# Performance work log

Measured on AMD Instinct MI355X. Metric: run time of the kernel, lower is better.

Reference implementation:

```python
import jax, jax.numpy as jnp
import numpy as np

N_NODES, N_EDGES, N_GRAPHS = 30000, 70000, 1024
TOWERS, F_IN, F_OUT, N_LAYERS = 5, 75, 15, 4
DEG_HIST = np.array([0.0, 100.0, 400.0, 300.0, 50.0], dtype=np.float32)
AVG_DEG_LOG = float((np.log(np.arange(len(DEG_HIST)) + 1.0) * DEG_HIST).sum() / DEG_HIST.sum())


def setup_inputs():
    key = jax.random.key(0)
    ks = jax.random.split(key, 16)
    g = lambda k, shp, fan: jax.random.normal(k, shp, jnp.float32) * (1.0 / np.sqrt(fan))
    return dict(
        x=jax.random.randint(ks[0], (N_NODES,), 0, 21),
        edge_index=jax.random.randint(ks[1], (2, N_EDGES), 0, N_NODES),
        edge_attr=jax.random.randint(ks[2], (N_EDGES,), 0, 4),
        batch=jnp.sort(jax.random.randint(ks[3], (N_NODES,), 0, N_GRAPHS)),
        node_emb=g(ks[4], (21, 75), 75),
        edge_emb=g(ks[5], (4, 50), 50),
        enc_w=g(ks[6], (N_LAYERS, 50, 75), 50),
        enc_b=jnp.zeros((N_LAYERS, 75), jnp.float32),
        pre_w=g(ks[7], (N_LAYERS, TOWERS, 3 * F_IN, F_IN), 3 * F_IN),
        pre_b=jnp.zeros((N_LAYERS, TOWERS, F_IN), jnp.float32),
        post_w=g(ks[8], (N_LAYERS, TOWERS, 13 * F_IN, F_OUT), 13 * F_IN),
        post_b=jnp.zeros((N_LAYERS, TOWERS, F_OUT), jnp.float32),
        lin_w=g(ks[9], (N_LAYERS, 75, 75), 75),
        lin_b=jnp.zeros((N_LAYERS, 75), jnp.float32),
        bn_g=jnp.ones((N_LAYERS, 75), jnp.float32),
        bn_b=jnp.zeros((N_LAYERS, 75), jnp.float32),
        mlp_w1=g(ks[10], (75, 50), 75), mlp_b1=jnp.zeros((50,), jnp.float32),
        mlp_w2=g(ks[11], (50, 25), 50), mlp_b2=jnp.zeros((25,), jnp.float32),
        mlp_w3=g(ks[12], (25, 1), 25), mlp_b3=jnp.zeros((1,), jnp.float32),
    )


def _pna_layer(h, src, dst, e_enc, pw, pb, qw, qb, lw, lb):
    n = h.shape[0]
    # message: cat[x_i, x_j, edge_enc] shared across towers, per-tower pre-NN
    msg = jnp.concatenate([h[dst], h[src], e_enc], axis=-1)            # [E, 3*F_in]
    m = jnp.einsum('ef,tfo->eto', msg, pw) + pb                        # [E, T, F_in]
    deg = jax.ops.segment_sum(jnp.ones((m.shape[0],), m.dtype), dst, n)
    has = (deg > 0)[:, None, None]
    cnt = jnp.maximum(deg, 1.0)[:, None, None]                         # clamp(1)
    mean = jax.ops.segment_sum(m, dst, n) / cnt
    mean_sq = jax.ops.segment_sum(m * m, dst, n) / cnt
    std = jnp.sqrt(jax.nn.relu(mean_sq - mean * mean) + 1e-5)
    mn = jnp.where(has, jax.ops.segment_min(m, dst, n), 0.0)
    mx = jnp.where(has, jax.ops.segment_max(m, dst, n), 0.0)
    agg = jnp.concatenate([mean, mn, mx, std], axis=-1)                # [N, T, 4*F_in]
    amp = jnp.log(cnt + 1.0) / AVG_DEG_LOG                             # amplification scaler
    scaled = jnp.concatenate([agg, agg * amp, agg / amp], axis=-1)     # [N, T, 12*F_in]
    post_in = jnp.concatenate(
        [jnp.broadcast_to(h[:, None, :], (n, TOWERS, F_IN)), scaled], axis=-1)  # [N, T, 13*F_in]
    out = jnp.einsum('ntf,tfo->nto', post_in, qw) + qb                 # [N, T, F_out]
    return out.reshape(n, TOWERS * F_OUT) @ lw + lb                    # [N, 75]


def _bn_relu(h, g, b):
    mu = h.mean(axis=0)
    var = h.var(axis=0)
    return jax.nn.relu((h - mu) * jax.lax.rsqrt(var + 1e-5) * g + b)


def reference(x, edge_index, edge_attr, batch, node_emb, edge_emb, enc_w, enc_b,
              pre_w, pre_b, post_w, post_b, lin_w, lin_b, bn_g, bn_b,
              mlp_w1, mlp_b1, mlp_w2, mlp_b2, mlp_w3, mlp_b3):
    h = node_emb[x]                      # [N, 75]
    e = edge_emb[edge_attr]              # [E, 50]
    src, dst = edge_index[0], edge_index[1]
    for l in range(N_LAYERS):
        e_enc = e @ enc_w[l] + enc_b[l]  # [E, 75]
        h = _bn_relu(_pna_layer(h, src, dst, e_enc, pre_w[l], pre_b[l],
                                post_w[l], post_b[l], lin_w[l], lin_b[l]),
                     bn_g[l], bn_b[l])
    hg = jax.ops.segment_sum(h, batch, N_GRAPHS)   # global_add_pool -> [G, 75]
    z = jax.nn.relu(hg @ mlp_w1 + mlp_b1)
    z = jax.nn.relu(z @ mlp_w2 + mlp_b2)
    return z @ mlp_w3 + mlp_b3
```

## Files before the change

kernel.cpp:

```cpp
#include <hip/hip_runtime.h>
#include <hip/hip_bf16.h>
#include <float.h>
#include <math.h>

#define NN 30000
#define NE 70000
#define NG 1024
#define NT 5
#define FI 75
#define NL 4

#define AMP_DENOM 1.1824939264481302f

#define ABW 832
#define AGW 1600
#define HBW 96
#define SBH 328

typedef __attribute__((ext_vector_type(8))) short bf16x8;
typedef __attribute__((ext_vector_type(4))) float f32x4;

__device__ __forceinline__ float bf2f(unsigned short u) {
    return __uint_as_float(((unsigned int)u) << 16);
}
__device__ __forceinline__ unsigned short f2bf(float f) {
    __hip_bfloat16 h = __float2bfloat16(f);
    return *reinterpret_cast<unsigned short*>(&h);
}

__global__ __launch_bounds__(256) void k_deg(const int* __restrict__ dst, int* __restrict__ deg) {
    int e = blockIdx.x * 256 + threadIdx.x;
    if (e < NE) atomicAdd(&deg[dst[e]], 1);
}

__global__ __launch_bounds__(1024) void k_scan(const int* __restrict__ deg, int* __restrict__ rowptr) {
    __shared__ int wsum[16];
    __shared__ int s_carry;
    int tid = threadIdx.x;
    int lane = tid & 63, wv = tid >> 6;
    if (tid == 0) s_carry = 0;
    __syncthreads();
    for (int base = 0; base < NN; base += 1024) {
        int i = base + tid;
        int v = (i < NN) ? deg[i] : 0;
        int x = v;
        #pragma unroll
        for (int off = 1; off < 64; off <<= 1) {
            int t = __shfl_up(x, off);
            if (lane >= off) x += t;
        }
        if (lane == 63) wsum[wv] = x;
        __syncthreads();
        if (tid < 16) {
            int y = wsum[tid];
            #pragma unroll
            for (int off = 1; off < 16; off <<= 1) {
                int t = __shfl_up(y, off);
                if (tid >= off) y += t;
            }
            wsum[tid] = y;
        }
        __syncthreads();
        int wbase = ((wv > 0) ? wsum[wv - 1] : 0) + s_carry;
        if (i < NN) rowptr[i] = wbase + x - v;
        int tot = wsum[15];
        __syncthreads();
        if (tid == 0) s_carry += tot;
    }
    __syncthreads();
    if (tid == 0) rowptr[NN] = s_carry;
}

__global__ __launch_bounds__(256) void k_scatter(const int* __restrict__ src, const int* __restrict__ dst,
                                                 const int* __restrict__ attr, const int* __restrict__ rowptr,
                                                 int* __restrict__ fill, int* __restrict__ csr) {
    int e = blockIdx.x * 256 + threadIdx.x;
    if (e < NE) {
        int d = dst[e];
        int pos = rowptr[d] + atomicAdd(&fill[d], 1);
        csr[pos] = src[e] | (attr[e] << 20);
    }
}

__global__ __launch_bounds__(256) void k_amp(const int* __restrict__ rowptr,
                                             float* __restrict__ amp, float* __restrict__ inv) {
    int n = blockIdx.x * 256 + threadIdx.x;
    if (n < NN) {
        int dg = rowptr[n + 1] - rowptr[n];
        float cnt = fmaxf((float)dg, 1.0f);
        float a = logf(cnt + 1.0f) * (1.0f / AMP_DENOM);
        amp[n] = a;
        inv[n] = 1.0f / a;
    }
}

__global__ __launch_bounds__(256) void k_h0(const int* __restrict__ x, const float* __restrict__ emb,
                                            unsigned short* __restrict__ hb) {
    int idx = blockIdx.x * 256 + threadIdx.x;
    if (idx < NN * HBW) {
        int n = idx / HBW, f = idx % HBW;
        hb[idx] = (f < FI) ? f2bf(emb[x[n] * FI + f]) : (unsigned short)0;
    }
}

__global__ __launch_bounds__(256) void k_wprep3(const float* __restrict__ post_w,
                                                unsigned short* __restrict__ Wpost2) {
    int idx = blockIdx.x * 256 + threadIdx.x;
    if (idx >= NL * NT * 3 * 16 * SBH) return;
    int kk = idx % SBH;
    int col = (idx / SBH) & 15;
    int s = (idx / (SBH * 16)) % 3;
    int t = (idx / (SBH * 16 * 3)) % NT;
    int l = idx / (SBH * 16 * 3 * NT);
    float val = 0.0f;
    if (kk < 304 && col < 15) {
        int stat = kk / 76, of = kk - stat * 76;
        if (of < 75)
            val = post_w[((size_t)(l * NT + t) * 975 + 75 + s * 300 + stat * 75 + of) * 15 + col];
    }
    Wpost2[idx] = f2bf(val);
}

__global__ __launch_bounds__(256) void k_wprep2(const float* __restrict__ pre_w,
                                                const float* __restrict__ post_w,
                                                unsigned short* __restrict__ WcatT) {
    int idx = blockIdx.x * 256 + threadIdx.x;
    if (idx >= NL * 832 * 96) return;
    int k = idx % 96;
    int j = (idx / 96) % 832;
    int l = idx / (96 * 832);
    float val = 0.0f;
    if (k < 75) {
        if (j < 375) {
            int t = j / 75, o = j % 75;
            val = pre_w[((size_t)(l * NT + t) * 225 + k) * FI + o];
        } else if (j < 750) {
            int jm = j - 375;
            int t = jm / 75, o = jm % 75;
            val = pre_w[((size_t)(l * NT + t) * 225 + 75 + k) * FI + o];
        } else if (j < 825) {
            int c = j - 750;
            int t = c / 15, o = c % 15;
            val = post_w[((size_t)(l * NT + t) * 975 + k) * 15 + o];
        }
    }
    WcatT[idx] = f2bf(val);
}

__global__ __launch_bounds__(256) void k_wprep4(const float* __restrict__ lin_w,
                                                unsigned short* __restrict__ linT) {
    int idx = blockIdx.x * 256 + threadIdx.x;
    if (idx >= NL * 80 * 96) return;
    int k = idx % 96;
    int c = (idx / 96) % 80;
    int l = idx / (96 * 80);
    float v = 0.0f;
    if (k < 75 && c < 75) v = lin_w[(size_t)l * 5625 + k * 75 + c];
    linT[idx] = f2bf(v);
}

__global__ __launch_bounds__(384) void k_tbl4(const float* __restrict__ edge_emb, const float* __restrict__ enc_w,
                                              const float* __restrict__ enc_b, const float* __restrict__ pre_w,
                                              const float* __restrict__ pre_b, float* __restrict__ tbl4) {
    __shared__ float e4[4][FI];
    int l = blockIdx.x;
    int tid = threadIdx.x;
    float* tbl = tbl4 + l * 1500;
    if (tid < 300) {
        int a = tid / FI, f = tid % FI;
        float acc = enc_b[l * FI + f];
        for (int k = 0; k < 50; k++)
            acc += edge_emb[a * 50 + k] * enc_w[(l * 50 + k) * FI + f];
        e4[a][f] = acc;
    }
    __syncthreads();
    for (int idx = tid; idx < 4 * 375; idx += 384) {
        int a = idx / 375, c = idx % 375;
        int t = c / FI, o = c % FI;
        const float* wp = pre_w + ((size_t)(l * NT + t) * 225 + 150) * FI + o;
        float acc = pre_b[(l * NT + t) * FI + o];
        for (int f = 0; f < FI; f++)
            acc += e4[a][f] * wp[f * FI];
        tbl[idx] = acc;
    }
}

__global__ __launch_bounds__(256) void k_preab(const unsigned short* __restrict__ hb,
                                               const float* __restrict__ zz,
                                               const float* __restrict__ bnsumP,
                                               const float* __restrict__ bngP,
                                               const float* __restrict__ bnbP,
                                               const unsigned short* __restrict__ WcatT,
                                               int l, __hip_bfloat16* __restrict__ ABH) {
    __shared__ __align__(16) unsigned short sA[128 * 104];
    __shared__ __align__(16) unsigned short sB[208 * 104];
    __shared__ float s_sc[75], s_sh[75];
    int tid = threadIdx.x;
    int m0 = blockIdx.x * 128;
    int j0 = blockIdx.y * 208;

    if (l > 0 && tid < 75) {
        float mu = bnsumP[tid] * (1.0f / NN);
        float msq = bnsumP[76 + tid] * (1.0f / NN);
        float var = msq - mu * mu;
        float sc = rsqrtf(var + 1e-5f) * bngP[tid];
        s_sc[tid] = sc;
        s_sh[tid] = bnbP[tid] - mu * sc;
    }
    const uint4* wsrc = (const uint4*)(WcatT + (size_t)l * 832 * 96);
    for (int c = tid; c < 208 * 12; c += 256) {
        int r = c / 12, q = c % 12;
        *(uint4*)&sB[r * 104 + q * 8] = wsrc[(size_t)(j0 + r) * 12 + q];
    }
    if (l == 0) {
        const uint4* hsrc = (const uint4*)hb;
        for (int c = tid; c < 128 * 12; c += 256) {
            int r = c / 12, q = c % 12;
            int n = m0 + r;
            uint4 v = make_uint4(0, 0, 0, 0);
            if (n < NN) v = hsrc[(size_t)n * 12 + q];
            *(uint4*)&sA[r * 104 + q * 8] = v;
        }
    } else {
        __syncthreads();
        for (int idx = tid; idx < 128 * 96; idx += 256) {
            int r = idx / 96, c = idx - (idx / 96) * 96;
            int n = m0 + r;
            float v = 0.0f;
            if (c < 75 && n < NN) {
                v = zz[(size_t)n * 75 + c];
                v = fmaxf(v * s_sc[c] + s_sh[c], 0.0f);
            }
            sA[r * 104 + c] = f2bf(v);
        }
    }
    __syncthreads();

    int w = tid >> 6, lane = tid & 63;
    int mw = w * 32;
    int lr = lane & 15, lq = lane >> 4;

    bf16x8 af[2][3];
    #pragma unroll
    for (int mt = 0; mt < 2; mt++)
        #pragma unroll
        for (int ks = 0; ks < 3; ks++)
            af[mt][ks] = *(const bf16x8*)&sA[(mw + mt * 16 + lr) * 104 + ks * 32 + lq * 8];

    f32x4 acc[13][2];
    #pragma unroll
    for (int nt = 0; nt < 13; nt++)
        #pragma unroll
        for (int mt = 0; mt < 2; mt++)
            acc[nt][mt] = (f32x4){0.0f, 0.0f, 0.0f, 0.0f};

    #pragma unroll
    for (int nt = 0; nt < 13; nt++) {
        #pragma unroll
        for (int ks = 0; ks < 3; ks++) {
            bf16x8 bf = *(const bf16x8*)&sB[(nt * 16 + lr) * 104 + ks * 32 + lq * 8];
            acc[nt][0] = __builtin_amdgcn_mfma_f32_16x16x32_bf16(af[0][ks], bf, acc[nt][0], 0, 0, 0);
            acc[nt][1] = __builtin_amdgcn_mfma_f32_16x16x32_bf16(af[1][ks], bf, acc[nt][1], 0, 0, 0);
        }
    }

    #pragma unroll
    for (int nt = 0; nt < 13; nt++) {
        int col = j0 + nt * 16 + lr;
        #pragma unroll
        for (int mt = 0; mt < 2; mt++) {
            #pragma unroll
            for (int r = 0; r < 4; r++) {
                int n = m0 + mw + mt * 16 + lq * 4 + r;
                if (n < NN) ABH[(size_t)n * ABW + col] = __float2bfloat16(acc[nt][mt][r]);
            }
        }
    }
}

__global__ __launch_bounds__(256) void k_gather(const __hip_bfloat16* __restrict__ ABH,
                                                const float* __restrict__ tbl,
                                                const int* __restrict__ rowptr, const int* __restrict__ csr,
                                                unsigned short* __restrict__ AGG) {
    __shared__ float s_tbl[1500];
    int tid = threadIdx.x;
    for (int i = tid; i < 1500; i += 256) s_tbl[i] = tbl[i];
    __syncthreads();

    int w = tid >> 6, l = tid & 63;
    int n = blockIdx.x * 4 + w;
    int base = rowptr[n];
    int dg = rowptr[n + 1] - base;

    float sum[6], ss[6], mn[6], mx[6];
    #pragma unroll
    for (int j = 0; j < 6; j++) { sum[j] = 0.f; ss[j] = 0.f; mn[j] = FLT_MAX; mx[j] = -FLT_MAX; }

    const unsigned short* abu = (const unsigned short*)ABH;
    int k = 0;
    for (; k + 1 < dg; k += 2) {
        int pk0 = csr[base + k], pk1 = csr[base + k + 1];
        const unsigned short* bp0 = abu + (size_t)(pk0 & 0xFFFFF) * ABW + 375;
        const unsigned short* bp1 = abu + (size_t)(pk1 & 0xFFFFF) * ABW + 375;
        const float* tp0 = s_tbl + (pk0 >> 20) * 375;
        const float* tp1 = s_tbl + (pk1 >> 20) * 375;
        #pragma unroll
        for (int j = 0; j < 6; j++) {
            int f = l + 64 * j;
            if (f < 375) {
                float v0 = bf2f(bp0[f]) + tp0[f];
                float v1 = bf2f(bp1[f]) + tp1[f];
                sum[j] += v0 + v1;
                ss[j] += v0 * v0 + v1 * v1;
                mn[j] = fminf(mn[j], fminf(v0, v1));
                mx[j] = fmaxf(mx[j], fmaxf(v0, v1));
            }
        }
    }
    if (k < dg) {
        int pk0 = csr[base + k];
        const unsigned short* bp0 = abu + (size_t)(pk0 & 0xFFFFF) * ABW + 375;
        const float* tp0 = s_tbl + (pk0 >> 20) * 375;
        #pragma unroll
        for (int j = 0; j < 6; j++) {
            int f = l + 64 * j;
            if (f < 375) {
                float v0 = bf2f(bp0[f]) + tp0[f];
                sum[j] += v0; ss[j] += v0 * v0;
                mn[j] = fminf(mn[j], v0); mx[j] = fmaxf(mx[j], v0);
            }
        }
    }

    unsigned short* out = AGG + (size_t)n * AGW;
    if (dg > 0) {
        float rc = 1.0f / (float)dg;
        const unsigned short* ap = abu + (size_t)n * ABW;
        #pragma unroll
        for (int j = 0; j < 6; j++) {
            int f = l + 64 * j;
            if (f < 375) {
                int t = f / 75, of = f - t * 75;
                int o = t * 320 + of;
                float Af = bf2f(ap[f]);
                float mean = sum[j] * rc;
                float var = ss[j] * rc - mean * mean;
                out[o]       = f2bf(Af + mean);
                out[o + 76]  = f2bf(Af + mn[j]);
                out[o + 152] = f2bf(Af + mx[j]);
                out[o + 228] = f2bf(sqrtf(fmaxf(var, 0.0f) + 1e-5f));
            }
        }
    } else {
        unsigned short zz = 0;
        unsigned short sd = f2bf(0.0031622776601683794f);
        #pragma unroll
        for (int j = 0; j < 6; j++) {
            int f = l + 64 * j;
            if (f < 375) {
                int t = f / 75, of = f - t * 75;
                int o = t * 320 + of;
                out[o] = zz; out[o + 76] = zz; out[o + 152] = zz; out[o + 228] = sd;
            }
        }
    }
    for (int i = l; i < 80; i += 64) out[(i >> 4) * 320 + 304 + (i & 15)] = 0;
    if (l < 20) out[(l >> 2) * 320 + (l & 3) * 76 + 75] = 0;
}

__global__ __launch_bounds__(256) void k_post(const __hip_bfloat16* __restrict__ ABH,
                                              const unsigned short* __restrict__ AGG,
                                              const unsigned short* __restrict__ Wpost2,
                                              const unsigned short* __restrict__ linT,
                                              const float* __restrict__ amp_a, const float* __restrict__ inv_a,
                                              const float* __restrict__ post_b, const float* __restrict__ lin_b,
                                              int l, float* __restrict__ z, float* __restrict__ bnsum) {
    __shared__ __align__(16) unsigned short s_y[128 * 96];
    __shared__ float s_bn[152];

    int tid = threadIdx.x;
    int n0 = blockIdx.x * 128;
    int w = tid >> 6, lane = tid & 63;
    int lr = lane & 15, lq = lane >> 4;
    int mw = w * 32;
    if (tid < 152) s_bn[tid] = 0.0f;
    for (int i = tid; i < 128 * 21; i += 256) {
        int r = i / 21, c = 75 + (i - (i / 21) * 21);
        s_y[r * 96 + c] = 0;
    }

    float am[2][4], iv[2][4];
    int rown[2][4];
    #pragma unroll
    for (int mt = 0; mt < 2; mt++)
        #pragma unroll
        for (int r = 0; r < 4; r++) {
            int n = n0 + mw + mt * 16 + lq * 4 + r;
            int nc = (n < NN) ? n : (NN - 1);
            rown[mt][r] = nc;
            am[mt][r] = amp_a[nc];
            iv[mt][r] = inv_a[nc];
        }
    int arow[2];
    #pragma unroll
    for (int mt = 0; mt < 2; mt++) {
        int n = n0 + mw + mt * 16 + lr;
        arow[mt] = (n < NN) ? n : (NN - 1);
    }

    const unsigned short* abu = (const unsigned short*)ABH;

    for (int t = 0; t < NT; t++) {
        const unsigned short* wt = Wpost2 + ((size_t)((l * NT + t) * 3 * 16) + lr) * SBH;
        const unsigned short* a0p = AGG + (size_t)arow[0] * AGW + t * 320;
        const unsigned short* a1p = AGG + (size_t)arow[1] * AGW + t * 320;

        f32x4 acc[2][3];
        #pragma unroll
        for (int mt = 0; mt < 2; mt++)
            #pragma unroll
            for (int s = 0; s < 3; s++)
                acc[mt][s] = (f32x4){0.0f, 0.0f, 0.0f, 0.0f};

        #pragma unroll
        for (int ks = 0; ks < 10; ks++) {
            int off = ks * 32 + lq * 8;
            bf16x8 b0 = *(const bf16x8*)&wt[off];
            bf16x8 b1 = *(const bf16x8*)&wt[16 * SBH + off];
            bf16x8 b2 = *(const bf16x8*)&wt[32 * SBH + off];
            bf16x8 a0 = *(const bf16x8*)&a0p[off];
            bf16x8 a1 = *(const bf16x8*)&a1p[off];
            acc[0][0] = __builtin_amdgcn_mfma_f32_16x16x32_bf16(a0, b0, acc[0][0], 0, 0, 0);
            acc[0][1] = __builtin_amdgcn_mfma_f32_16x16x32_bf16(a0, b1, acc[0][1], 0, 0, 0);
            acc[0][2] = __builtin_amdgcn_mfma_f32_16x16x32_bf16(a0, b2, acc[0][2], 0, 0, 0);
            acc[1][0] = __builtin_amdgcn_mfma_f32_16x16x32_bf16(a1, b0, acc[1][0], 0, 0, 0);
            acc[1][1] = __builtin_amdgcn_mfma_f32_16x16x32_bf16(a1, b1, acc[1][1], 0, 0, 0);
            acc[1][2] = __builtin_amdgcn_mfma_f32_16x16x32_bf16(a1, b2, acc[1][2], 0, 0, 0);
        }

        if (lr < 15) {
            float qb = post_b[(l * NT + t) * 15 + lr];
            #pragma unroll
            for (int mt = 0; mt < 2; mt++)
                #pragma unroll
                for (int r = 0; r < 4; r++) {
                    float ht = bf2f(abu[(size_t)rown[mt][r] * ABW + 750 + t * 15 + lr]);
                    float y = acc[mt][0][r] + am[mt][r] * acc[mt][1][r] + iv[mt][r] * acc[mt][2][r] + ht + qb;
                    s_y[(mw + mt * 16 + lq * 4 + r) * 96 + t * 15 + lr] = f2bf(y);
                }
        }
    }
    __syncthreads();

    const unsigned short* lt = linT + (size_t)l * 80 * 96;
    bf16x8 af[2][3];
    #pragma unroll
    for (int mt = 0; mt < 2; mt++)
        #pragma unroll
        for (int ks = 0; ks < 3; ks++)
            af[mt][ks] = *(const bf16x8*)&s_y[(mw + mt * 16 + lr) * 96 + ks * 32 + lq * 8];

    f32x4 acc2[5][2];
    #pragma unroll
    for (int nt = 0; nt < 5; nt++)
        #pragma unroll
        for (int mt = 0; mt < 2; mt++)
            acc2[nt][mt] = (f32x4){0.0f, 0.0f, 0.0f, 0.0f};

    #pragma unroll
    for (int nt = 0; nt < 5; nt++) {
        #pragma unroll
        for (int ks = 0; ks < 3; ks++) {
            bf16x8 bf = *(const bf16x8*)&lt[(nt * 16 + lr) * 96 + ks * 32 + lq * 8];
            acc2[nt][0] = __builtin_amdgcn_mfma_f32_16x16x32_bf16(af[0][ks], bf, acc2[nt][0], 0, 0, 0);
            acc2[nt][1] = __builtin_amdgcn_mfma_f32_16x16x32_bf16(af[1][ks], bf, acc2[nt][1], 0, 0, 0);
        }
    }

    float b1a[5] = {}, b2a[5] = {};
    #pragma unroll
    for (int nt = 0; nt < 5; nt++) {
        int c = nt * 16 + lr;
        bool cv = (c < 75);
        float lb = cv ? lin_b[l * 75 + c] : 0.0f;
        #pragma unroll
        for (int mt = 0; mt < 2; mt++)
            #pragma unroll
            for (int r = 0; r < 4; r++) {
                int n = n0 + mw + mt * 16 + lq * 4 + r;
                if (cv && n < NN) {
                    float v = acc2[nt][mt][r] + lb;
                    z[(size_t)n * 75 + c] = v;
                    b1a[nt] += v;
                    b2a[nt] += v * v;
                }
            }
    }
    #pragma unroll
    for (int nt = 0; nt < 5; nt++) {
        b1a[nt] += __shfl_xor(b1a[nt], 16); b1a[nt] += __shfl_xor(b1a[nt], 32);
        b2a[nt] += __shfl_xor(b2a[nt], 16); b2a[nt] += __shfl_xor(b2a[nt], 32);
    }
    if (lq == 0) {
        #pragma unroll
        for (int nt = 0; nt < 5; nt++) {
            int c = nt * 16 + lr;
            if (c < 75) {
                atomicAdd(&s_bn[c], b1a[nt]);
                atomicAdd(&s_bn[76 + c], b2a[nt]);
            }
        }
    }
    __syncthreads();
    if (tid < 75) {
        atomicAdd(&bnsum[tid], s_bn[tid]);
        atomicAdd(&bnsum[76 + tid], s_bn[76 + tid]);
    }
}

__global__ __launch_bounds__(256) void k_pool(const float* __restrict__ z, const float* __restrict__ bnsum3,
                                              const float* __restrict__ bng, const float* __restrict__ bnb,
                                              const int* __restrict__ batch, float* __restrict__ hg) {
    __shared__ float s_sc[75], s_sh[75];
    int tid = threadIdx.x;
    if (tid < 75) {
        float mu = bnsum3[tid] * (1.0f / NN);
        float msq = bnsum3[76 + tid] * (1.0f / NN);
        float var = msq - mu * mu;
        float sc = rsqrtf(var + 1e-5f) * bng[tid];
        s_sc[tid] = sc;
        s_sh[tid] = bnb[tid] - mu * sc;
    }
    __syncthreads();
    int idx = blockIdx.x * 256 + tid;
    if (idx < NN * 75) {
        int n = idx / 75, f = idx % 75;
        float v = fmaxf(z[idx] * s_sc[f] + s_sh[f], 0.0f);
        atomicAdd(&hg[batch[n] * 75 + f], v);
    }
}

__global__ __launch_bounds__(64) void k_mlp(const float* __restrict__ hg,
                                            const float* __restrict__ w1, const float* __restrict__ b1,
                                            const float* __restrict__ w2, const float* __restrict__ b2,
                                            const float* __restrict__ w3, const float* __restrict__ b3,
                                            float* __restrict__ out) {
    __shared__ float zin[75], z1[50], z2[25];
    int g = blockIdx.x, tid = threadIdx.x;
    for (int k = tid; k < 75; k += 64) zin[k] = hg[g * 75 + k];
    __syncthreads();
    if (tid < 50) {
        float acc = b1[tid];
        for (int k = 0; k < 75; k++) acc += zin[k] * w1[k * 50 + tid];
        z1[tid] = fmaxf(acc, 0.0f);
    }
    __syncthreads();
    if (tid < 25) {
        float acc = b2[tid];
        for (int k = 0; k < 50; k++) acc += z1[k] * w2[k * 25 + tid];
        z2[tid] = fmaxf(acc, 0.0f);
    }
    __syncthreads();
    if (tid == 0) {
        float acc = b3[0];
        for (int k = 0; k < 25; k++) acc += z2[k] * w3[k];
        out[g] = acc;
    }
}

extern "C" void kernel_launch(void* const* d_in, const int* in_sizes, int n_in,
                              void* d_out, int out_size, void* d_ws, size_t ws_size,
                              hipStream_t stream) {
    const int* x        = (const int*)d_in[0];
    const int* ei       = (const int*)d_in[1];
    const int* eattr    = (const int*)d_in[2];
    const int* batch    = (const int*)d_in[3];
    const float* node_emb = (const float*)d_in[4];
    const float* edge_emb = (const float*)d_in[5];
    const float* enc_w  = (const float*)d_in[6];
    const float* enc_b  = (const float*)d_in[7];
    const float* pre_w  = (const float*)d_in[8];
    const float* pre_b  = (const float*)d_in[9];
    const float* post_w = (const float*)d_in[10];
    const float* post_b = (const float*)d_in[11];
    const float* lin_w  = (const float*)d_in[12];
    const float* lin_b  = (const float*)d_in[13];
    const float* bn_g   = (const float*)d_in[14];
    const float* bn_b   = (const float*)d_in[15];
    const float* w1     = (const float*)d_in[16];
    const float* b1     = (const float*)d_in[17];
    const float* w2     = (const float*)d_in[18];
    const float* b2     = (const float*)d_in[19];
    const float* w3     = (const float*)d_in[20];
    const float* b3     = (const float*)d_in[21];

    char* p = (char*)d_ws;
    auto carve = [&](size_t bytes) -> char* {
        char* r = p;
        p += ((bytes + 255) & ~(size_t)255);
        return r;
    };
    __hip_bfloat16* ABH = (__hip_bfloat16*)carve((size_t)NN * ABW * 2);
    unsigned short* AGG = (unsigned short*)carve((size_t)NN * AGW * 2);
    float* z     = (float*)carve((size_t)NN * 75 * 4);
    unsigned short* hb = (unsigned short*)carve((size_t)NN * HBW * 2);
    unsigned short* WcatT = (unsigned short*)carve((size_t)NL * 832 * 96 * 2);
    unsigned short* Wpost2 = (unsigned short*)carve((size_t)NL * NT * 3 * 16 * SBH * 2);
    unsigned short* linT = (unsigned short*)carve((size_t)NL * 80 * 96 * 2);
    float* tbl4  = (float*)carve((size_t)NL * 1500 * 4);
    int* deg     = (int*)carve(NN * 4);
    int* rowptr  = (int*)carve((NN + 1) * 4);
    int* fill    = (int*)carve(NN * 4);
    int* csr     = (int*)carve(NE * 4);
    float* bnsum = (float*)carve((size_t)NL * 152 * 4);
    float* amp_a = (float*)carve(NN * 4);
    float* inv_a = (float*)carve(NN * 4);
    float* hg    = (float*)carve((size_t)NG * 75 * 4);

    hipMemsetAsync(deg, 0, NN * 4, stream);
    hipMemsetAsync(fill, 0, NN * 4, stream);
    hipMemsetAsync(hg, 0, (size_t)NG * 75 * 4, stream);
    hipMemsetAsync(bnsum, 0, (size_t)NL * 152 * 4, stream);

    k_deg<<<(NE + 255) / 256, 256, 0, stream>>>(ei + NE, deg);
    k_scan<<<1, 1024, 0, stream>>>(deg, rowptr);
    k_scatter<<<(NE + 255) / 256, 256, 0, stream>>>(ei, ei + NE, eattr, rowptr, fill, csr);
    k_amp<<<(NN + 255) / 256, 256, 0, stream>>>(rowptr, amp_a, inv_a);
    k_h0<<<(NN * HBW + 255) / 256, 256, 0, stream>>>(x, node_emb, hb);
    k_wprep3<<<(NL * NT * 3 * 16 * SBH + 255) / 256, 256, 0, stream>>>(post_w, Wpost2);
    k_wprep2<<<(NL * 832 * 96 + 255) / 256, 256, 0, stream>>>(pre_w, post_w, WcatT);
    k_wprep4<<<(NL * 80 * 96 + 255) / 256, 256, 0, stream>>>(lin_w, linT);
    k_tbl4<<<NL, 384, 0, stream>>>(edge_emb, enc_w, enc_b, pre_w, pre_b, tbl4);

    for (int l = 0; l < NL; l++) {
        k_preab<<<dim3((NN + 127) / 128, 4), 256, 0, stream>>>(
            hb, z, bnsum + (l > 0 ? (l - 1) * 152 : 0),
            bn_g + (l > 0 ? (l - 1) * 75 : 0), bn_b + (l > 0 ? (l - 1) * 75 : 0),
            WcatT, l, ABH);
        k_gather<<<NN / 4, 256, 0, stream>>>(ABH, tbl4 + l * 1500, rowptr, csr, AGG);
        k_post<<<(NN + 127) / 128, 256, 0, stream>>>(ABH, AGG, Wpost2, linT, amp_a, inv_a,
                                                     post_b, lin_b, l, z, bnsum + l * 152);
    }

    k_pool<<<(NN * 75 + 255) / 256, 256, 0, stream>>>(z, bnsum + 3 * 152, bn_g + 3 * 75, bn_b + 3 * 75,
                                                      batch, hg);
    k_mlp<<<NG, 64, 0, stream>>>(hg, w1, b1, w2, b2, w3, b3, (float*)d_out);
}
```

Baseline: 583.1 us.

## Fuse neighbor gather/aggregation into post-MLP kernel and split BN into separate pass

The separate gather kernel, which wrote the per-node aggregate buffer (AGG) to global memory, is merged into the post-NN kernel (k_fgp). Each block now aggregates neighbor statistics per tower into shared memory and immediately runs the MFMA post and linear GEMMs, removing the large AGG round trip. Weights are pre-swizzled into MFMA lane order, and the BN+ReLU prologue moves out of k_preab into a standalone elementwise kernel, which adds an extra pass over z and hb. The gather now uses one wave per 16 nodes serially per tower, which may reduce memory-level parallelism in the irregular neighbor loads.

```diff
diff --git a/kernel.cpp b/kernel.cpp
--- a/kernel.cpp
+++ b/kernel.cpp
@@ -13,9 +13,8 @@
 #define AMP_DENOM 1.1824939264481302f
 
 #define ABW 832
-#define AGW 1600
 #define HBW 96
-#define SBH 328
+#define ZW 76
 
 typedef __attribute__((ext_vector_type(8))) short bf16x8;
 typedef __attribute__((ext_vector_type(4))) float f32x4;
@@ -103,22 +102,25 @@
     }
 }
 
-__global__ __launch_bounds__(256) void k_wprep3(const float* __restrict__ post_w,
-                                                unsigned short* __restrict__ Wpost2) {
+__global__ __launch_bounds__(256) void k_wprep5(const float* __restrict__ post_w,
+                                                unsigned short* __restrict__ Wp5) {
     int idx = blockIdx.x * 256 + threadIdx.x;
-    if (idx >= NL * NT * 3 * 16 * SBH) return;
-    int kk = idx % SBH;
-    int col = (idx / SBH) & 15;
-    int s = (idx / (SBH * 16)) % 3;
-    int t = (idx / (SBH * 16 * 3)) % NT;
-    int l = idx / (SBH * 16 * 3 * NT);
+    if (idx >= NL * NT * 3 * 10 * 512) return;
+    int e = idx & 7;
+    int lane = (idx >> 3) & 63;
+    int ks = (idx >> 9) % 10;
+    int s = (idx / 5120) % 3;
+    int t = (idx / 15360) % NT;
+    int l = idx / 76800;
+    int lr = lane & 15, lq = lane >> 4;
+    int kk = ks * 32 + lq * 8 + e;
     float val = 0.0f;
-    if (kk < 304 && col < 15) {
+    if (kk < 304 && lr < 15) {
         int stat = kk / 76, of = kk - stat * 76;
         if (of < 75)
-            val = post_w[((size_t)(l * NT + t) * 975 + 75 + s * 300 + stat * 75 + of) * 15 + col];
-    }
-    Wpost2[idx] = f2bf(val);
+            val = post_w[((size_t)(l * NT + t) * 975 + 75 + s * 300 + stat * 75 + of) * 15 + lr];
+    }
+    Wp5[idx] = f2bf(val);
 }
 
 __global__ __launch_bounds__(256) void k_wprep2(const float* __restrict__ pre_w,
@@ -148,15 +150,20 @@
 }
 
 __global__ __launch_bounds__(256) void k_wprep4(const float* __restrict__ lin_w,
-                                                unsigned short* __restrict__ linT) {
+                                                unsigned short* __restrict__ linTp) {
     int idx = blockIdx.x * 256 + threadIdx.x;
-    if (idx >= NL * 80 * 96) return;
-    int k = idx % 96;
-    int c = (idx / 96) % 80;
-    int l = idx / (96 * 80);
+    if (idx >= NL * 5 * 3 * 512) return;
+    int e = idx & 7;
+    int lane = (idx >> 3) & 63;
+    int ks = (idx >> 9) % 3;
+    int nt = (idx / 1536) % 5;
+    int l = idx / 7680;
+    int lr = lane & 15, lq = lane >> 4;
+    int c = nt * 16 + lr;
+    int k = ks * 32 + lq * 8 + e;
     float v = 0.0f;
     if (k < 75 && c < 75) v = lin_w[(size_t)l * 5625 + k * 75 + c];
-    linT[idx] = f2bf(v);
+    linTp[idx] = f2bf(v);
 }
 
 __global__ __launch_bounds__(384) void k_tbl4(const float* __restrict__ edge_emb, const float* __restrict__ enc_w,
@@ -185,55 +192,51 @@
     }
 }
 
+__global__ __launch_bounds__(256) void k_bnh(const float* __restrict__ z, const float* __restrict__ bnsum,
+                                             const float* __restrict__ bng, const float* __restrict__ bnb,
+                                             unsigned short* __restrict__ hb) {
+    __shared__ float s_sc[75], s_sh[75];
+    int tid = threadIdx.x;
+    if (tid < 75) {
+        float mu = bnsum[tid] * (1.0f / NN);
+        float msq = bnsum[76 + tid] * (1.0f / NN);
+        float var = msq - mu * mu;
+        float sc = rsqrtf(var + 1e-5f) * bng[tid];
+        s_sc[tid] = sc;
+        s_sh[tid] = bnb[tid] - mu * sc;
+    }
+    __syncthreads();
+    int idx = blockIdx.x * 256 + tid;
+    if (idx < NN * HBW) {
+        int n = idx / HBW, c = idx % HBW;
+        float v = 0.0f;
+        if (c < 75) v = fmaxf(z[(size_t)n * ZW + c] * s_sc[c] + s_sh[c], 0.0f);
+        hb[idx] = (c < 75) ? f2bf(v) : (unsigned short)0;
+    }
+}
+
 __global__ __launch_bounds__(256) void k_preab(const unsigned short* __restrict__ hb,
-                                               const float* __restrict__ zz,
-                                               const float* __restrict__ bnsumP,
-                                               const float* __restrict__ bngP,
-                                               const float* __restrict__ bnbP,
                                                const unsigned short* __restrict__ WcatT,
                                                int l, __hip_bfloat16* __restrict__ ABH) {
     __shared__ __align__(16) unsigned short sA[128 * 104];
     __shared__ __align__(16) unsigned short sB[208 * 104];
-    __shared__ float s_sc[75], s_sh[75];
     int tid = threadIdx.x;
     int m0 = blockIdx.x * 128;
     int j0 = blockIdx.y * 208;
 
-    if (l > 0 && tid < 75) {
-        float mu = bnsumP[tid] * (1.0f / NN);
-        float msq = bnsumP[76 + tid] * (1.0f / NN);
-        float var = msq - mu * mu;
-        float sc = rsqrtf(var + 1e-5f) * bngP[tid];
-        s_sc[tid] = sc;
-        s_sh[tid] = bnbP[tid] - mu * sc;
+    const uint4* hsrc = (const uint4*)hb;
+    for (int c = tid; c < 128 * 12; c += 256) {
+        int r = c / 12, q = c % 12;
+        int n = m0 + r;
+        uint4 v = make_uint4(0, 0, 0, 0);
+        if (n < NN) v = hsrc[(size_t)n * 12 + q];
+        *(uint4*)&sA[r * 104 + q * 8] = v;
     }
     const uint4* wsrc = (const uint4*)(WcatT + (size_t)l * 832 * 96);
     for (int c = tid; c < 208 * 12; c += 256) {
         int r = c / 12, q = c % 12;
         *(uint4*)&sB[r * 104 + q * 8] = wsrc[(size_t)(j0 + r) * 12 + q];
     }
-    if (l == 0) {
-        const uint4* hsrc = (const uint4*)hb;
-        for (int c = tid; c < 128 * 12; c += 256) {
-            int r = c / 12, q = c % 12;
-            int n = m0 + r;
-            uint4 v = make_uint4(0, 0, 0, 0);
-            if (n < NN) v = hsrc[(size_t)n * 12 + q];
-            *(uint4*)&sA[r * 104 + q * 8] = v;
-        }
-    } else {
-        __syncthreads();
-        for (int idx = tid; idx < 128 * 96; idx += 256) {
-            int r = idx / 96, c = idx - (idx / 96) * 96;
-            int n = m0 + r;
-            float v = 0.0f;
-            if (c < 75 && n < NN) {
-                v = zz[(size_t)n * 75 + c];
-                v = fmaxf(v * s_sc[c] + s_sh[c], 0.0f);
-            }
-            sA[r * 104 + c] = f2bf(v);
-        }
-    }
     __syncthreads();
 
     int w = tid >> 6, lane = tid & 63;
@@ -259,255 +262,216 @@
         #pragma unroll
         for (int ks = 0; ks < 3; ks++) {
             bf16x8 bf = *(const bf16x8*)&sB[(nt * 16 + lr) * 104 + ks * 32 + lq * 8];
-            acc[nt][0] = __builtin_amdgcn_mfma_f32_16x16x32_bf16(af[0][ks], bf, acc[nt][0], 0, 0, 0);
-            acc[nt][1] = __builtin_amdgcn_mfma_f32_16x16x32_bf16(af[1][ks], bf, acc[nt][1], 0, 0, 0);
-        }
-    }
-
+            acc[nt][0] = __builtin_amdgcn_mfma_f32_16x16x32_bf16(bf, af[0][ks], acc[nt][0], 0, 0, 0);
+            acc[nt][1] = __builtin_amdgcn_mfma_f32_16x16x32_bf16(bf, af[1][ks], acc[nt][1], 0, 0, 0);
+        }
+    }
+
+    unsigned short* abo = (unsigned short*)ABH;
     #pragma unroll
-    for (int nt = 0; nt < 13; nt++) {
-        int col = j0 + nt * 16 + lr;
-        #pragma unroll
-        for (int mt = 0; mt < 2; mt++) {
+    for (int mt = 0; mt < 2; mt++) {
+        int n = m0 + mw + mt * 16 + lr;
+        if (n < NN) {
+            #pragma unroll
+            for (int nt = 0; nt < 13; nt++) {
+                int c0 = j0 + nt * 16 + lq * 4;
+                ushort4 us;
+                us.x = f2bf(acc[nt][mt][0]);
+                us.y = f2bf(acc[nt][mt][1]);
+                us.z = f2bf(acc[nt][mt][2]);
+                us.w = f2bf(acc[nt][mt][3]);
+                *(ushort4*)&abo[(size_t)n * ABW + c0] = us;
+            }
+        }
+    }
+}
+
+__global__ __launch_bounds__(256) void k_fgp(const __hip_bfloat16* __restrict__ ABH,
+                                             const float* __restrict__ tbl,
+                                             const int* __restrict__ rowptr, const int* __restrict__ csr,
+                                             const unsigned short* __restrict__ Wp5,
+                                             const unsigned short* __restrict__ linTp,
+                                             const float* __restrict__ amp_a, const float* __restrict__ inv_a,
+                                             const float* __restrict__ post_b, const float* __restrict__ lin_b,
+                                             int l, float* __restrict__ z, float* __restrict__ bnsum) {
+    __shared__ __align__(16) unsigned short s_agg[64 * 328];
+    __shared__ __align__(16) unsigned short s_y[64 * 104];
+    __shared__ float s_tbl2[304];
+    __shared__ float s_bn[152];
+
+    int tid = threadIdx.x;
+    int n0 = blockIdx.x * 64;
+    int w = tid >> 6, lane = tid & 63;
+    int lr = lane & 15, lq = lane >> 4;
+
+    if (tid < 152) s_bn[tid] = 0.0f;
+    for (int i = tid; i < 64 * 28; i += 256) {
+        int r = i / 28, c = i % 28;
+        int col = (c < 4) ? (c * 76 + 75) : (300 + c);
+        s_agg[r * 328 + col] = 0;
+    }
+    for (int i = tid; i < 64 * 29; i += 256) {
+        int r = i / 29, c = 75 + i % 29;
+        s_y[r * 104 + c] = 0;
+    }
+
+    const unsigned short* abu = (const unsigned short*)ABH;
+    int mynode = n0 + w * 16 + lr;
+    int mclamp = (mynode < NN) ? mynode : (NN - 1);
+    float amp = amp_a[mclamp], inv = inv_a[mclamp];
+
+    int f0 = lane;
+    bool h1 = (lane < 11);
+    int f1 = h1 ? (64 + lane) : 74;
+
+    for (int t = 0; t < NT; t++) {
+        for (int i = tid; i < 304; i += 256) {
+            int a = i / 76, f = i % 76;
+            s_tbl2[i] = (f < 75) ? tbl[a * 375 + t * 75 + f] : 0.0f;
+        }
+        __syncthreads();
+
+        for (int ni = 0; ni < 16; ni++) {
+            int node = n0 + w * 16 + ni;
+            unsigned short* ag = &s_agg[(w * 16 + ni) * 328];
+            int base = 0, dg = 0;
+            if (node < NN) {
+                base = rowptr[node];
+                dg = rowptr[node + 1] - base;
+            }
+            if (dg > 0) {
+                float sum0 = 0, ss0 = 0, mn0 = FLT_MAX, mx0 = -FLT_MAX;
+                float sum1 = 0, ss1 = 0, mn1 = FLT_MAX, mx1 = -FLT_MAX;
+                int k2 = 0;
+                while (k2 < dg) {
+                    int pk[4]; unsigned short rv0[4], rv1[4];
+                    #pragma unroll
+                    for (int j = 0; j < 4; j++) {
+                        int kk = k2 + j; kk = (kk < dg) ? kk : (dg - 1);
+                        pk[j] = csr[base + kk];
+                    }
+                    #pragma unroll
+                    for (int j = 0; j < 4; j++) {
+                        const unsigned short* bp = abu + (size_t)(pk[j] & 0xFFFFF) * ABW + 375 + t * 75;
+                        rv0[j] = bp[f0];
+                        rv1[j] = bp[f1];
+                    }
+                    int cnt = dg - k2; cnt = (cnt < 4) ? cnt : 4;
+                    #pragma unroll
+                    for (int j = 0; j < 4; j++) {
+                        if (j < cnt) {
+                            const float* tp = s_tbl2 + (pk[j] >> 20) * 76;
+                            float v0 = bf2f(rv0[j]) + tp[f0];
+                            float v1 = bf2f(rv1[j]) + tp[f1];
+                            sum0 += v0; ss0 += v0 * v0; mn0 = fminf(mn0, v0); mx0 = fmaxf(mx0, v0);
+                            sum1 += v1; ss1 += v1 * v1; mn1 = fminf(mn1, v1); mx1 = fmaxf(mx1, v1);
+                        }
+                    }
+                    k2 += 4;
+                }
+                float rc = 1.0f / (float)dg;
+                {
+                    float Af = bf2f(abu[(size_t)node * ABW + t * 75 + f0]);
+                    float mean = sum0 * rc;
+                    float var = ss0 * rc - mean * mean;
+                    ag[f0]       = f2bf(Af + mean);
+                    ag[76 + f0]  = f2bf(Af + mn0);
+                    ag[152 + f0] = f2bf(Af + mx0);
+                    ag[228 + f0] = f2bf(sqrtf(fmaxf(var, 0.0f) + 1e-5f));
+                }
+                if (h1) {
+                    float Af = bf2f(abu[(size_t)node * ABW + t * 75 + f1]);
+                    float mean = sum1 * rc;
+                    float var = ss1 * rc - mean * mean;
+                    ag[f1]       = f2bf(Af + mean);
+                    ag[76 + f1]  = f2bf(Af + mn1);
+                    ag[152 + f1] = f2bf(Af + mx1);
+                    ag[228 + f1] = f2bf(sqrtf(fmaxf(var, 0.0f) + 1e-5f));
+                }
+            } else {
+                unsigned short sd = f2bf(0.0031622776601683794f);
+                ag[f0] = 0; ag[76 + f0] = 0; ag[152 + f0] = 0; ag[228 + f0] = sd;
+                if (h1) { ag[f1] = 0; ag[76 + f1] = 0; ag[152 + f1] = 0; ag[228 + f1] = sd; }
+            }
+        }
+        __syncthreads();
+
+        const unsigned short* wp = Wp5 + (size_t)(l * NT + t) * 3 * 10 * 512;
+        const unsigned short* arow = &s_agg[(w * 16 + lr) * 328];
+        f32x4 ac0 = {0, 0, 0, 0}, ac1 = {0, 0, 0, 0}, ac2 = {0, 0, 0, 0};
+        #pragma unroll
+        for (int ks = 0; ks < 10; ks++) {
+            bf16x8 a = *(const bf16x8*)&arow[ks * 32 + lq * 8];
+            bf16x8 b0 = *(const bf16x8*)&wp[(0 * 10 + ks) * 512 + lane * 8];
+            bf16x8 b1 = *(const bf16x8*)&wp[(1 * 10 + ks) * 512 + lane * 8];
+            bf16x8 b2 = *(const bf16x8*)&wp[(2 * 10 + ks) * 512 + lane * 8];
+            ac0 = __builtin_amdgcn_mfma_f32_16x16x32_bf16(b0, a, ac0, 0, 0, 0);
+            ac1 = __builtin_amdgcn_mfma_f32_16x16x32_bf16(b1, a, ac1, 0, 0, 0);
+            ac2 = __builtin_amdgcn_mfma_f32_16x16x32_bf16(b2, a, ac2, 0, 0, 0);
+        }
+        #pragma unroll
+        for (int r = 0; r < 4; r++) {
+            int f = lq * 4 + r;
+            if (f < 15) {
+                float qb = post_b[(l * NT + t) * 15 + f];
+                float ht = bf2f(abu[(size_t)mclamp * ABW + 750 + t * 15 + f]);
+                float y = ac0[r] + amp * ac1[r] + inv * ac2[r] + ht + qb;
+                s_y[(w * 16 + lr) * 104 + t * 15 + f] = f2bf(y);
+            }
+        }
+    }
+    __syncthreads();
+
+    const unsigned short* lp = linTp + (size_t)l * 5 * 3 * 512;
+    bf16x8 ya[3];
+    #pragma unroll
+    for (int ks = 0; ks < 3; ks++)
+        ya[ks] = *(const bf16x8*)&s_y[(w * 16 + lr) * 104 + ks * 32 + lq * 8];
+
+    #pragma unroll
+    for (int nt = 0; nt < 5; nt++) {
+        f32x4 a2 = {0, 0, 0, 0};
+        #pragma unroll
+        for (int ks = 0; ks < 3; ks++) {
+            bf16x8 bb = *(const bf16x8*)&lp[(nt * 3 + ks) * 512 + lane * 8];
+            a2 = __builtin_amdgcn_mfma_f32_16x16x32_bf16(bb, ya[ks], a2, 0, 0, 0);
+        }
+        int c0 = nt * 16 + lq * 4;
+        float v[4], vm[4], vm2[4];
+        #pragma unroll
+        for (int r = 0; r < 4; r++) {
+            int c = c0 + r;
+            v[r] = (c < 75) ? (a2[r] + lin_b[l * 75 + c]) : 0.0f;
+            bool ok = (c < 75) && (mynode < NN);
+            vm[r] = ok ? v[r] : 0.0f;
+            vm2[r] = ok ? v[r] * v[r] : 0.0f;
+        }
+        if (mynode < NN) {
+            if (c0 + 3 < 75) {
+                float4 st = make_float4(v[0], v[1], v[2], v[3]);
+                *(float4*)&z[(size_t)mynode * ZW + c0] = st;
+            } else {
+                #pragma unroll
+                for (int r = 0; r < 4; r++)
+                    if (c0 + r < 75) z[(size_t)mynode * ZW + c0 + r] = v[r];
+            }
+        }
+        #pragma unroll
+        for (int r = 0; r < 4; r++) {
+            #pragma unroll
+            for (int off = 1; off < 16; off <<= 1) {
+                vm[r] += __shfl_xor(vm[r], off);
+                vm2[r] += __shfl_xor(vm2[r], off);
+            }
+        }
+        if (lr == 0) {
             #pragma unroll
             for (int r = 0; r < 4; r++) {
-                int n = m0 + mw + mt * 16 + lq * 4 + r;
-                if (n < NN) ABH[(size_t)n * ABW + col] = __float2bfloat16(acc[nt][mt][r]);
-            }
-        }
-    }
-}
-
-__global__ __launch_bounds__(256) void k_gather(const __hip_bfloat16* __restrict__ ABH,
-                                                const float* __restrict__ tbl,
-                                                const int* __restrict__ rowptr, const int* __restrict__ csr,
-                                                unsigned short* __restrict__ AGG) {
-    __shared__ float s_tbl[1500];
-    int tid = threadIdx.x;
-    for (int i = tid; i < 1500; i += 256) s_tbl[i] = tbl[i];
-    __syncthreads();
-
-    int w = tid >> 6, l = tid & 63;
-    int n = blockIdx.x * 4 + w;
-    int base = rowptr[n];
-    int dg = rowptr[n + 1] - base;
-
-    float sum[6], ss[6], mn[6], mx[6];
-    #pragma unroll
-    for (int j = 0; j < 6; j++) { sum[j] = 0.f; ss[j] = 0.f; mn[j] = FLT_MAX; mx[j] = -FLT_MAX; }
-
-    const unsigned short* abu = (const unsigned short*)ABH;
-    int k = 0;
-    for (; k + 1 < dg; k += 2) {
-        int pk0 = csr[base + k], pk1 = csr[base + k + 1];
-        const unsigned short* bp0 = abu + (size_t)(pk0 & 0xFFFFF) * ABW + 375;
-        const unsigned short* bp1 = abu + (size_t)(pk1 & 0xFFFFF) * ABW + 375;
-        const float* tp0 = s_tbl + (pk0 >> 20) * 375;
-        const float* tp1 = s_tbl + (pk1 >> 20) * 375;
-        #pragma unroll
-        for (int j = 0; j < 6; j++) {
-            int f = l + 64 * j;
-            if (f < 375) {
-                float v0 = bf2f(bp0[f]) + tp0[f];
-                float v1 = bf2f(bp1[f]) + tp1[f];
-                sum[j] += v0 + v1;
-                ss[j] += v0 * v0 + v1 * v1;
-                mn[j] = fminf(mn[j], fminf(v0, v1));
-                mx[j] = fmaxf(mx[j], fmaxf(v0, v1));
-            }
-        }
-    }
-    if (k < dg) {
-        int pk0 = csr[base + k];
-        const unsigned short* bp0 = abu + (size_t)(pk0 & 0xFFFFF) * ABW + 375;
-        const float* tp0 = s_tbl + (pk0 >> 20) * 375;
-        #pragma unroll
-        for (int j = 0; j < 6; j++) {
-            int f = l + 64 * j;
-            if (f < 375) {
-                float v0 = bf2f(bp0[f]) + tp0[f];
-                sum[j] += v0; ss[j] += v0 * v0;
-                mn[j] = fminf(mn[j], v0); mx[j] = fmaxf(mx[j], v0);
-            }
-        }
-    }
-
-    unsigned short* out = AGG + (size_t)n * AGW;
-    if (dg > 0) {
-        float rc = 1.0f / (float)dg;
-        const unsigned short* ap = abu + (size_t)n * ABW;
-        #pragma unroll
-        for (int j = 0; j < 6; j++) {
-            int f = l + 64 * j;
-            if (f < 375) {
-                int t = f / 75, of = f - t * 75;
-                int o = t * 320 + of;
-                float Af = bf2f(ap[f]);
-                float mean = sum[j] * rc;
-                float var = ss[j] * rc - mean * mean;
-                out[o]       = f2bf(Af + mean);
-                out[o + 76]  = f2bf(Af + mn[j]);
-                out[o + 152] = f2bf(Af + mx[j]);
-                out[o + 228] = f2bf(sqrtf(fmaxf(var, 0.0f) + 1e-5f));
-            }
-        }
-    } else {
-        unsigned short zz = 0;
-        unsigned short sd = f2bf(0.0031622776601683794f);
-        #pragma unroll
-        for (int j = 0; j < 6; j++) {
-            int f = l + 64 * j;
-            if (f < 375) {
-                int t = f / 75, of = f - t * 75;
-                int o = t * 320 + of;
-                out[o] = zz; out[o + 76] = zz; out[o + 152] = zz; out[o + 228] = sd;
-            }
-        }
-    }
-    for (int i = l; i < 80; i += 64) out[(i >> 4) * 320 + 304 + (i & 15)] = 0;
-    if (l < 20) out[(l >> 2) * 320 + (l & 3) * 76 + 75] = 0;
-}
-
-__global__ __launch_bounds__(256) void k_post(const __hip_bfloat16* __restrict__ ABH,
-                                              const unsigned short* __restrict__ AGG,
-                                              const unsigned short* __restrict__ Wpost2,
-                                              const unsigned short* __restrict__ linT,
-                                              const float* __restrict__ amp_a, const float* __restrict__ inv_a,
-                                              const float* __restrict__ post_b, const float* __restrict__ lin_b,
-                                              int l, float* __restrict__ z, float* __restrict__ bnsum) {
-    __shared__ __align__(16) unsigned short s_y[128 * 96];
-    __shared__ float s_bn[152];
-
-    int tid = threadIdx.x;
-    int n0 = blockIdx.x * 128;
-    int w = tid >> 6, lane = tid & 63;
-    int lr = lane & 15, lq = lane >> 4;
-    int mw = w * 32;
-    if (tid < 152) s_bn[tid] = 0.0f;
-    for (int i = tid; i < 128 * 21; i += 256) {
-        int r = i / 21, c = 75 + (i - (i / 21) * 21);
-        s_y[r * 96 + c] = 0;
-    }
-
-    float am[2][4], iv[2][4];
-    int rown[2][4];
-    #pragma unroll
-    for (int mt = 0; mt < 2; mt++)
-        #pragma unroll
-        for (int r = 0; r < 4; r++) {
-            int n = n0 + mw + mt * 16 + lq * 4 + r;
-            int nc = (n < NN) ? n : (NN - 1);
-            rown[mt][r] = nc;
-            am[mt][r] = amp_a[nc];
-            iv[mt][r] = inv_a[nc];
-        }
-    int arow[2];
-    #pragma unroll
-    for (int mt = 0; mt < 2; mt++) {
-        int n = n0 + mw + mt * 16 + lr;
-        arow[mt] = (n < NN) ? n : (NN - 1);
-    }
-
-    const unsigned short* abu = (const unsigned short*)ABH;
-
-    for (int t = 0; t < NT; t++) {
-        const unsigned short* wt = Wpost2 + ((size_t)((l * NT + t) * 3 * 16) + lr) * SBH;
-        const unsigned short* a0p = AGG + (size_t)arow[0] * AGW + t * 320;
-        const unsigned short* a1p = AGG + (size_t)arow[1] * AGW + t * 320;
-
-        f32x4 acc[2][3];
-        #pragma unroll
-        for (int mt = 0; mt < 2; mt++)
-            #pragma unroll
-            for (int s = 0; s < 3; s++)
-                acc[mt][s] = (f32x4){0.0f, 0.0f, 0.0f, 0.0f};
-
-        #pragma unroll
-        for (int ks = 0; ks < 10; ks++) {
-            int off = ks * 32 + lq * 8;
-            bf16x8 b0 = *(const bf16x8*)&wt[off];
-            bf16x8 b1 = *(const bf16x8*)&wt[16 * SBH + off];
-            bf16x8 b2 = *(const bf16x8*)&wt[32 * SBH + off];
-            bf16x8 a0 = *(const bf16x8*)&a0p[off];
-            bf16x8 a1 = *(const bf16x8*)&a1p[off];
-            acc[0][0] = __builtin_amdgcn_mfma_f32_16x16x32_bf16(a0, b0, acc[0][0], 0, 0, 0);
-            acc[0][1] = __builtin_amdgcn_mfma_f32_16x16x32_bf16(a0, b1, acc[0][1], 0, 0, 0);
-            acc[0][2] = __builtin_amdgcn_mfma_f32_16x16x32_bf16(a0, b2, acc[0][2], 0, 0, 0);
-            acc[1][0] = __builtin_amdgcn_mfma_f32_16x16x32_bf16(a1, b0, acc[1][0], 0, 0, 0);
-            acc[1][1] = __builtin_amdgcn_mfma_f32_16x16x32_bf16(a1, b1, acc[1][1], 0, 0, 0);
-            acc[1][2] = __builtin_amdgcn_mfma_f32_16x16x32_bf16(a1, b2, acc[1][2], 0, 0, 0);
-        }
-
-        if (lr < 15) {
-            float qb = post_b[(l * NT + t) * 15 + lr];
-            #pragma unroll
-            for (int mt = 0; mt < 2; mt++)
-                #pragma unroll
-                for (int r = 0; r < 4; r++) {
-                    float ht = bf2f(abu[(size_t)rown[mt][r] * ABW + 750 + t * 15 + lr]);
-                    float y = acc[mt][0][r] + am[mt][r] * acc[mt][1][r] + iv[mt][r] * acc[mt][2][r] + ht + qb;
-                    s_y[(mw + mt * 16 + lq * 4 + r) * 96 + t * 15 + lr] = f2bf(y);
+                int c = c0 + r;
+                if (c < 75) {
+                    atomicAdd(&s_bn[c], vm[r]);
+                    atomicAdd(&s_bn[76 + c], vm2[r]);
                 }
-        }
-    }
-    __syncthreads();
-
-    const unsigned short* lt = linT + (size_t)l * 80 * 96;
-    bf16x8 af[2][3];
-    #pragma unroll
-    for (int mt = 0; mt < 2; mt++)
-        #pragma unroll
-        for (int ks = 0; ks < 3; ks++)
-            af[mt][ks] = *(const bf16x8*)&s_y[(mw + mt * 16 + lr) * 96 + ks * 32 + lq * 8];
-
-    f32x4 acc2[5][2];
-    #pragma unroll
-    for (int nt = 0; nt < 5; nt++)
-        #pragma unroll
-        for (int mt = 0; mt < 2; mt++)
-            acc2[nt][mt] = (f32x4){0.0f, 0.0f, 0.0f, 0.0f};
-
-    #pragma unroll
-    for (int nt = 0; nt < 5; nt++) {
-        #pragma unroll
-        for (int ks = 0; ks < 3; ks++) {
-            bf16x8 bf = *(const bf16x8*)&lt[(nt * 16 + lr) * 96 + ks * 32 + lq * 8];
-            acc2[nt][0] = __builtin_amdgcn_mfma_f32_16x16x32_bf16(af[0][ks], bf, acc2[nt][0], 0, 0, 0);
-            acc2[nt][1] = __builtin_amdgcn_mfma_f32_16x16x32_bf16(af[1][ks], bf, acc2[nt][1], 0, 0, 0);
-        }
-    }
-
-    float b1a[5] = {}, b2a[5] = {};
-    #pragma unroll
-    for (int nt = 0; nt < 5; nt++) {
-        int c = nt * 16 + lr;
-        bool cv = (c < 75);
-        float lb = cv ? lin_b[l * 75 + c] : 0.0f;
-        #pragma unroll
-        for (int mt = 0; mt < 2; mt++)
-            #pragma unroll
-            for (int r = 0; r < 4; r++) {
-                int n = n0 + mw + mt * 16 + lq * 4 + r;
-                if (cv && n < NN) {
-                    float v = acc2[nt][mt][r] + lb;
-                    z[(size_t)n * 75 + c] = v;
-                    b1a[nt] += v;
-                    b2a[nt] += v * v;
-                }
-            }
-    }
-    #pragma unroll
-    for (int nt = 0; nt < 5; nt++) {
-        b1a[nt] += __shfl_xor(b1a[nt], 16); b1a[nt] += __shfl_xor(b1a[nt], 32);
-        b2a[nt] += __shfl_xor(b2a[nt], 16); b2a[nt] += __shfl_xor(b2a[nt], 32);
-    }
-    if (lq == 0) {
-        #pragma unroll
-        for (int nt = 0; nt < 5; nt++) {
-            int c = nt * 16 + lr;
-            if (c < 75) {
-                atomicAdd(&s_bn[c], b1a[nt]);
-                atomicAdd(&s_bn[76 + c], b2a[nt]);
             }
         }
     }
@@ -535,7 +499,7 @@
     int idx = blockIdx.x * 256 + tid;
     if (idx < NN * 75) {
         int n = idx / 75, f = idx % 75;
-        float v = fmaxf(z[idx] * s_sc[f] + s_sh[f], 0.0f);
+        float v = fmaxf(z[(size_t)n * ZW + f] * s_sc[f] + s_sh[f], 0.0f);
         atomicAdd(&hg[batch[n] * 75 + f], v);
     }
 }
@@ -601,12 +565,11 @@
         return r;
     };
     __hip_bfloat16* ABH = (__hip_bfloat16*)carve((size_t)NN * ABW * 2);
-    unsigned short* AGG = (unsigned short*)carve((size_t)NN * AGW * 2);
-    float* z     = (float*)carve((size_t)NN * 75 * 4);
+    float* z     = (float*)carve((size_t)NN * ZW * 4);
     unsigned short* hb = (unsigned short*)carve((size_t)NN * HBW * 2);
     unsigned short* WcatT = (unsigned short*)carve((size_t)NL * 832 * 96 * 2);
-    unsigned short* Wpost2 = (unsigned short*)carve((size_t)NL * NT * 3 * 16 * SBH * 2);
-    unsigned short* linT = (unsigned short*)carve((size_t)NL * 80 * 96 * 2);
+    unsigned short* Wp5   = (unsigned short*)carve((size_t)NL * NT * 3 * 10 * 512 * 2);
+    unsigned short* linTp = (unsigned short*)carve((size_t)NL * 5 * 3 * 512 * 2);
     float* tbl4  = (float*)carve((size_t)NL * 1500 * 4);
     int* deg     = (int*)carve(NN * 4);
     int* rowptr  = (int*)carve((NN + 1) * 4);
@@ -627,19 +590,18 @@
     k_scatter<<<(NE + 255) / 256, 256, 0, stream>>>(ei, ei + NE, eattr, rowptr, fill, csr);
     k_amp<<<(NN + 255) / 256, 256, 0, stream>>>(rowptr, amp_a, inv_a);
     k_h0<<<(NN * HBW + 255) / 256, 256, 0, stream>>>(x, node_emb, hb);
-    k_wprep3<<<(NL * NT * 3 * 16 * SBH + 255) / 256, 256, 0, stream>>>(post_w, Wpost2);
+    k_wprep5<<<(NL * NT * 3 * 10 * 512 + 255) / 256, 256, 0, stream>>>(post_w, Wp5);
     k_wprep2<<<(NL * 832 * 96 + 255) / 256, 256, 0, stream>>>(pre_w, post_w, WcatT);
-    k_wprep4<<<(NL * 80 * 96 + 255) / 256, 256, 0, stream>>>(lin_w, linT);
+    k_wprep4<<<(NL * 5 * 3 * 512 + 255) / 256, 256, 0, stream>>>(lin_w, linTp);
     k_tbl4<<<NL, 384, 0, stream>>>(edge_emb, enc_w, enc_b, pre_w, pre_b, tbl4);
 
     for (int l = 0; l < NL; l++) {
-        k_preab<<<dim3((NN + 127) / 128, 4), 256, 0, stream>>>(
-            hb, z, bnsum + (l > 0 ? (l - 1) * 152 : 0),
-            bn_g + (l > 0 ? (l - 1) * 75 : 0), bn_b + (l > 0 ? (l - 1) * 75 : 0),
-            WcatT, l, ABH);
-        k_gather<<<NN / 4, 256, 0, stream>>>(ABH, tbl4 + l * 1500, rowptr, csr, AGG);
-        k_post<<<(NN + 127) / 128, 256, 0, stream>>>(ABH, AGG, Wpost2, linT, amp_a, inv_a,
-                                                     post_b, lin_b, l, z, bnsum + l * 152);
+        if (l > 0)
+            k_bnh<<<(NN * HBW + 255) / 256, 256, 0, stream>>>(
+                z, bnsum + (l - 1) * 152, bn_g + (l - 1) * 75, bn_b + (l - 1) * 75, hb);
+        k_preab<<<dim3((NN + 127) / 128, 4), 256, 0, stream>>>(hb, WcatT, l, ABH);
+        k_fgp<<<(NN + 63) / 64, 256, 0, stream>>>(ABH, tbl4 + l * 1500, rowptr, csr, Wp5, linTp,
+                                                  amp_a, inv_a, post_b, lin_b, l, z, bnsum + l * 152);
     }
 
     k_pool<<<(NN * 75 + 255) / 256, 256, 0, stream>>>(z, bnsum + 3 * 152, bn_g + 3 * 75, bn_b + 3 * 75,
```

New measurement: 1.035 ms. 77.5% more time.
